# Optimization experiments

Hardware: AMD Instinct MI355X
Metric: run time of the kernel (lower is better)

Reference implementation:

```python
import jax, jax.numpy as jnp
import numpy as np

B, T, N, D, NH = 4, 256, 8, 128, 4
SCALES = (1, 2, 3, 5)
LAGS = (1, 2, 3)
MLP_H = 32
NL_SCALE = 0.1
CMIN, CMAX = -2.5, 2.0
L_ENC = 2  # num_attn_layers


def _ln(x, g, b, eps=1e-5):
    m = x.mean(-1, keepdims=True)
    v = ((x - m) ** 2).mean(-1, keepdims=True)
    return (x - m) * jax.lax.rsqrt(v + eps) * g + b


def _gelu(x):
    return jax.nn.gelu(x, approximate=False)


def _mha(q, k, v, Wq, bq, Wk, bk, Wv, bv, Wo, bo, nh):
    Bq, Lq, Dm = q.shape
    Lk = k.shape[1]
    hd = Dm // nh
    qh = (q @ Wq.T + bq).reshape(Bq, Lq, nh, hd).transpose(0, 2, 1, 3)
    kh = (k @ Wk.T + bk).reshape(Bq, Lk, nh, hd).transpose(0, 2, 1, 3)
    vh = (v @ Wv.T + bv).reshape(Bq, Lk, nh, hd).transpose(0, 2, 1, 3)
    s = jnp.einsum('bhqd,bhkd->bhqk', qh, kh) / jnp.sqrt(jnp.float32(hd))
    p = jax.nn.softmax(s, axis=-1)
    o = jnp.einsum('bhqk,bhkd->bhqd', p, vh).transpose(0, 2, 1, 3).reshape(Bq, Lq, Dm)
    return o @ Wo.T + bo


def setup_inputs() -> dict:
    key = jax.random.key(0)
    ks = jax.random.split(key, 24)
    def w(k, shape, s=0.02):
        return s * jax.random.normal(k, shape, jnp.float32)
    inp = {}
    inp['visible_states'] = jax.random.uniform(ks[0], (B, T, N), jnp.float32) + 0.05
    inp['state_emb'] = jax.random.normal(ks[1], (B, T, N, D), jnp.float32)
    # LearnedBaseline params
    inp['r5'] = 0.1 * jnp.ones((N,), jnp.float32)
    A = 0.02 * jax.random.normal(ks[2], (N, N), jnp.float32)
    inp['A55'] = A.at[jnp.arange(N), jnp.arange(N)].set(-0.2)
    inp['bl_bias'] = jnp.zeros((N,), jnp.float32)
    inp['nl_W1'] = w(ks[3], (MLP_H, N), 0.1); inp['nl_b1'] = jnp.zeros((MLP_H,), jnp.float32)
    inp['nl_W2'] = w(ks[4], (N, MLP_H), 0.1); inp['nl_b2'] = jnp.zeros((N,), jnp.float32)
    # ResidualEncoder input MLP
    IN_DIM = len(SCALES) * (1 + len(LAGS))  # 16
    inp['mlp_W1'] = w(ks[5], (D, IN_DIM), 0.1); inp['mlp_b1'] = jnp.zeros((D,), jnp.float32)
    inp['mlp_W2'] = w(ks[6], (D, D)); inp['mlp_b2'] = jnp.zeros((D,), jnp.float32)
    inp['mlp_ln_g'] = jnp.ones((D,), jnp.float32); inp['mlp_ln_b'] = jnp.zeros((D,), jnp.float32)
    # ResidualEncoder transformer layers (stacked over L_ENC layers)
    inp['enc_qkv_W'] = w(ks[7], (L_ENC, 3 * D, D)); inp['enc_qkv_b'] = jnp.zeros((L_ENC, 3 * D), jnp.float32)
    inp['enc_out_W'] = w(ks[8], (L_ENC, D, D)); inp['enc_out_b'] = jnp.zeros((L_ENC, D), jnp.float32)
    inp['enc_ln1_g'] = jnp.ones((L_ENC, D), jnp.float32); inp['enc_ln1_b'] = jnp.zeros((L_ENC, D), jnp.float32)
    inp['enc_ff_W1'] = w(ks[9], (L_ENC, 2 * D, D)); inp['enc_ff_b1'] = jnp.zeros((L_ENC, 2 * D), jnp.float32)
    inp['enc_ff_W2'] = w(ks[10], (L_ENC, D, 2 * D)); inp['enc_ff_b2'] = jnp.zeros((L_ENC, D), jnp.float32)
    inp['enc_ln2_g'] = jnp.ones((L_ENC, D), jnp.float32); inp['enc_ln2_b'] = jnp.zeros((L_ENC, D), jnp.float32)
    # CrossAttentionFusion
    inp['ca_Wq'] = w(ks[11], (D, D)); inp['ca_bq'] = jnp.zeros((D,), jnp.float32)
    inp['ca_Wk'] = w(ks[12], (D, D)); inp['ca_bk'] = jnp.zeros((D,), jnp.float32)
    inp['ca_Wv'] = w(ks[13], (D, D)); inp['ca_bv'] = jnp.zeros((D,), jnp.float32)
    inp['ca_Wo'] = w(ks[14], (D, D)); inp['ca_bo'] = jnp.zeros((D,), jnp.float32)
    inp['ca_ln1_g'] = jnp.ones((D,), jnp.float32); inp['ca_ln1_b'] = jnp.zeros((D,), jnp.float32)
    inp['ca_ff_W1'] = w(ks[15], (4 * D, 2 * D)); inp['ca_ff_b1'] = jnp.zeros((4 * D,), jnp.float32)
    inp['ca_ff_W2'] = w(ks[16], (D, 4 * D)); inp['ca_ff_b2'] = jnp.zeros((D,), jnp.float32)
    inp['ca_ln2_g'] = jnp.ones((D,), jnp.float32); inp['ca_ln2_b'] = jnp.zeros((D,), jnp.float32)
    return inp


def _forward(visible_states, state_emb, r5, A55, bl_bias, nl_W1, nl_b1, nl_W2, nl_b2,
             mlp_W1, mlp_b1, mlp_W2, mlp_b2, mlp_ln_g, mlp_ln_b,
             enc_qkv_W, enc_qkv_b, enc_out_W, enc_out_b, enc_ln1_g, enc_ln1_b,
             enc_ff_W1, enc_ff_b1, enc_ff_W2, enc_ff_b2, enc_ln2_g, enc_ln2_b,
             ca_Wq, ca_bq, ca_Wk, ca_bk, ca_Wv, ca_bv, ca_Wo, ca_bo,
             ca_ln1_g, ca_ln1_b, ca_ff_W1, ca_ff_b1, ca_ff_W2, ca_ff_b2,
             ca_ln2_g, ca_ln2_b):
    # ---- LearnedBaseline on x_t = visible_states[:, :-1] ----
    safe = jnp.clip(visible_states, 1e-6, None)
    logx = jnp.log(safe)
    x_t = visible_states[:, :-1]  # (B,T-1,N)
    lin = r5 + jnp.einsum('btn,mn->btm', x_t, A55)
    nl = _gelu(x_t @ nl_W1.T + nl_b1) @ nl_W2.T + nl_b2
    b1 = lin + NL_SCALE * nl + bl_bias  # (B,T-1,N)
    # ---- MultiScaleResidual ----
    res_list = []
    for k in SCALES:
        actual = jnp.clip(logx[:, k:] - logx[:, :-k], CMIN * k, CMAX * k)  # (B,T-k,N)
        bk = b1[:, 0:T - k]
        for i in range(1, k):
            bk = bk + b1[:, i:i + T - k]
        res = actual - bk
        res_list.append(jnp.pad(res, ((0, 0), (0, k), (0, 0))))
    residuals = jnp.stack(res_list, axis=-1)  # (B,T,N,S)
    # ---- ResidualEncoder: takens delays ----
    feats = [residuals] + [jnp.pad(residuals, ((0, 0), (lag, 0), (0, 0), (0, 0)))[:, :T]
                           for lag in LAGS]
    x = jnp.concatenate(feats, axis=-1)  # (B,T,N,16)
    x = _gelu(x @ mlp_W1.T + mlp_b1)
    x = _gelu(x @ mlp_W2.T + mlp_b2)
    x = _ln(x, mlp_ln_g, mlp_ln_b)
    # sinusoidal PE over time
    pos = jnp.arange(T, dtype=jnp.float32)[:, None]
    div = jnp.exp(jnp.arange(0, D, 2, dtype=jnp.float32) * (-jnp.log(10000.0) / D))
    pe = jnp.stack([jnp.sin(pos * div), jnp.cos(pos * div)], axis=-1).reshape(T, D)
    x = x + pe[None, :, None, :]
    # temporal self-attention over (B*N, T, D)
    xt = x.transpose(0, 2, 1, 3).reshape(B * N, T, D)
    for i in range(L_ENC):
        Wq, Wk, Wv = jnp.split(enc_qkv_W[i], 3, axis=0)
        bq, bk_, bv = jnp.split(enc_qkv_b[i], 3)
        a = _mha(xt, xt, xt, Wq, bq, Wk, bk_, Wv, bv, enc_out_W[i], enc_out_b[i], NH)
        xt = _ln(xt + a, enc_ln1_g[i], enc_ln1_b[i])
        ff = _gelu(xt @ enc_ff_W1[i].T + enc_ff_b1[i]) @ enc_ff_W2[i].T + enc_ff_b2[i]
        xt = _ln(xt + ff, enc_ln2_g[i], enc_ln2_b[i])
    residual_emb = xt.reshape(B, N, T, D).transpose(0, 2, 1, 3)  # (B,T,N,D)
    # ---- CrossAttentionFusion ----
    s = state_emb.reshape(B, T * N, D)
    r = residual_emb.reshape(B, T * N, D)
    a = _mha(s, r, r, ca_Wq, ca_bq, ca_Wk, ca_bk, ca_Wv, ca_bv, ca_Wo, ca_bo, NH)
    s = _ln(s + a, ca_ln1_g, ca_ln1_b)
    fused = _gelu(jnp.concatenate([s, r], axis=-1) @ ca_ff_W1.T + ca_ff_b1) @ ca_ff_W2.T + ca_ff_b2
    out = _ln(s + fused, ca_ln2_g, ca_ln2_b)
    return out.reshape(B, T, N, D)


def reference(visible_states, state_emb, r5, A55, bl_bias, nl_W1, nl_b1, nl_W2, nl_b2,
              mlp_W1, mlp_b1, mlp_W2, mlp_b2, mlp_ln_g, mlp_ln_b,
              enc_qkv_W, enc_qkv_b, enc_out_W, enc_out_b, enc_ln1_g, enc_ln1_b,
              enc_ff_W1, enc_ff_b1, enc_ff_W2, enc_ff_b2, enc_ln2_g, enc_ln2_b,
              ca_Wq, ca_bq, ca_Wk, ca_bk, ca_Wv, ca_bv, ca_Wo, ca_bo,
              ca_ln1_g, ca_ln1_b, ca_ff_W1, ca_ff_b1, ca_ff_W2, ca_ff_b2,
              ca_ln2_g, ca_ln2_b):
    return _forward(visible_states, state_emb, r5, A55, bl_bias, nl_W1, nl_b1, nl_W2, nl_b2,
                    mlp_W1, mlp_b1, mlp_W2, mlp_b2, mlp_ln_g, mlp_ln_b,
                    enc_qkv_W, enc_qkv_b, enc_out_W, enc_out_b, enc_ln1_g, enc_ln1_b,
                    enc_ff_W1, enc_ff_b1, enc_ff_W2, enc_ff_b2, enc_ln2_g, enc_ln2_b,
                    ca_Wq, ca_bq, ca_Wk, ca_bk, ca_Wv, ca_bv, ca_Wo, ca_bo,
                    ca_ln1_g, ca_ln1_b, ca_ff_W1, ca_ff_b1, ca_ff_W2, ca_ff_b2,
                    ca_ln2_g, ca_ln2_b)
```

## Files before the change

kernel.cpp:

```cpp
#include <hip/hip_runtime.h>
#include <math.h>

#define B_ 4
#define T_ 256
#define N_ 8
#define D_ 128
#define NH_ 4
#define HD_ 32
#define LENC_ 2
#define MLPH_ 32
#define NL_SCALE_ 0.1f

typedef __bf16 bf16;
typedef __attribute__((ext_vector_type(2))) __bf16 bf16x2;
typedef __attribute__((ext_vector_type(4))) __bf16 bf16x4;
typedef __attribute__((ext_vector_type(8))) __bf16 bf16x8;
typedef __attribute__((ext_vector_type(4))) float f32x4;

__device__ __forceinline__ f32x4 pv_mfma16(bf16x4 a, bf16x4 b, f32x4 c) {
#if __has_builtin(__builtin_amdgcn_mfma_f32_16x16x16_bf16)
    return __builtin_amdgcn_mfma_f32_16x16x16_bf16(a, b, c, 0, 0, 0);
#else
    typedef __attribute__((ext_vector_type(4))) short s4;
    union U { bf16x4 h; s4 s; };
    U ua, ub; ua.h = a; ub.h = b;
    return __builtin_amdgcn_mfma_f32_16x16x16bf16_1k(ua.s, ub.s, c, 0, 0, 0);
#endif
}

__device__ __forceinline__ float gelu_f(float x) {
    return 0.5f * x * (1.0f + erff(x * 0.7071067811865476f));
}

__device__ __forceinline__ float exp2_fast(float x) {
#if __has_builtin(__builtin_amdgcn_exp2f)
    return __builtin_amdgcn_exp2f(x);
#else
    return __expf(x * 0.6931471805599453f);
#endif
}

#define SCALE_LOG2E 0.25503486f

__global__ void k_prep_b1(const float* __restrict__ eqkvW, const float* __restrict__ eoutW,
                          const float* __restrict__ eff1, const float* __restrict__ eff2,
                          const float* __restrict__ wq, const float* __restrict__ wk,
                          const float* __restrict__ wv, const float* __restrict__ wo,
                          const float* __restrict__ cff1, const float* __restrict__ cff2,
                          const float* __restrict__ mlpW2, const float* __restrict__ semb,
                          const float* __restrict__ bk, const float* __restrict__ bv,
                          bf16* __restrict__ Wpk, bf16* __restrict__ sembh,
                          float* __restrict__ bpk,
                          const float* __restrict__ vs, const float* __restrict__ r5,
                          const float* __restrict__ A55, const float* __restrict__ bl_bias,
                          const float* __restrict__ nlW1, const float* __restrict__ nlb1,
                          const float* __restrict__ nlW2, const float* __restrict__ nlb2,
                          float* __restrict__ b1w) {
    if (blockIdx.x < 6209) {
        int i = blockIdx.x * 256 + threadIdx.x;
        if (i < 540672) {
            const float* src; int off;
            if      (i < 98304)  { src = eqkvW; off = 0; }
            else if (i < 131072) { src = eoutW; off = 98304; }
            else if (i < 196608) { src = eff1;  off = 131072; }
            else if (i < 262144) { src = eff2;  off = 196608; }
            else if (i < 278528) { src = wq;    off = 262144; }
            else if (i < 294912) { src = wk;    off = 278528; }
            else if (i < 311296) { src = wv;    off = 294912; }
            else if (i < 327680) { src = wo;    off = 311296; }
            else if (i < 458752) { src = cff1;  off = 327680; }
            else if (i < 524288) { src = cff2;  off = 458752; }
            else                 { src = mlpW2; off = 524288; }
            Wpk[i] = (bf16)src[i - off];
        } else if (i < 540672 + 1048576) {
            int j = i - 540672;
            sembh[j] = (bf16)semb[j];
        } else if (i < 540672 + 1048576 + 256) {
            int t = i - 540672 - 1048576;
            bpk[t] = (t < 128) ? bk[t] : bv[t - 128];
        }
        return;
    }
    int idx = (blockIdx.x - 6209) * 256 + threadIdx.x;
    if (idx >= B_ * (T_ - 1)) return;
    int b = idx / (T_ - 1), t = idx % (T_ - 1);
    float x[N_];
    for (int n = 0; n < N_; n++) x[n] = vs[(b * T_ + t) * N_ + n];
    float h[MLPH_];
    for (int j = 0; j < MLPH_; j++) {
        float a = nlb1[j];
        for (int n = 0; n < N_; n++) a += x[n] * nlW1[j * N_ + n];
        h[j] = gelu_f(a);
    }
    for (int m = 0; m < N_; m++) {
        float lin = r5[m];
        for (int n = 0; n < N_; n++) lin += x[n] * A55[m * N_ + n];
        float nl = nlb2[m];
        for (int j = 0; j < MLPH_; j++) nl += h[j] * nlW2[m * MLPH_ + j];
        b1w[idx * N_ + m] = lin + NL_SCALE_ * nl + bl_bias[m];
    }
}

__global__ __launch_bounds__(256) void k_mlp_ln(
    const float* __restrict__ vs, const float* __restrict__ b1w,
    const float* __restrict__ W1, const float* __restrict__ b1,
    const bf16* __restrict__ W2, const float* __restrict__ bias,
    const float* __restrict__ g, const float* __restrict__ be,
    float* __restrict__ outf, bf16* __restrict__ outh) {
    __shared__ float F[16][16];
    __shared__ bf16 H1[16][136];
    __shared__ float S[16][132];
    int tid = threadIdx.x;
    int blk = blockIdx.x;
    {
        int row = tid >> 4, feat = tid & 15;
        int grow = blk * 16 + row;
        int b = grow >> 11, t = (grow >> 3) & 255, n = grow & 7;
        const int SC[4] = {1, 2, 3, 5};
        int lag = feat >> 2, si = feat & 3, k = SC[si];
        int tp = t - lag;
        float r = 0.0f;
        if (tp >= 0 && tp < T_ - k) {
            float lx0 = logf(fmaxf(vs[(b * T_ + tp) * N_ + n], 1e-6f));
            float lx1 = logf(fmaxf(vs[(b * T_ + tp + k) * N_ + n], 1e-6f));
            float a = lx1 - lx0;
            a = fminf(fmaxf(a, -2.5f * (float)k), 2.0f * (float)k);
            float bk = 0.0f;
            for (int i = 0; i < k; i++) bk += b1w[(b * (T_ - 1) + tp + i) * N_ + n];
            r = a - bk;
        }
        F[row][feat] = r;
    }
    __syncthreads();
    {
        int row = tid >> 4, cg = tid & 15;
        float f[16];
#pragma unroll
        for (int c = 0; c < 16; c++) f[c] = F[row][c];
#pragma unroll
        for (int j = 0; j < 8; j++) {
            int d = cg * 8 + j;
            float a = b1[d];
            const float* w = W1 + d * 16;
#pragma unroll
            for (int c = 0; c < 16; c++) a += f[c] * w[c];
            H1[row][d] = (bf16)gelu_f(a);
        }
    }
    __syncthreads();
    int w = tid >> 6, lane = tid & 63;
    int c = lane & 15, gq = lane >> 4;
    int cb = w * 32;
    const f32x4 zero = {0, 0, 0, 0};
    {
        const bf16x8* Wp0 = (const bf16x8*)(W2 + (size_t)(cb + c) * 128) + gq;
        const bf16x8* Wp1 = (const bf16x8*)(W2 + (size_t)(cb + 16 + c) * 128) + gq;
        f32x4 a0 = zero, a1 = zero;
#pragma unroll
        for (int k = 0; k < 4; k++) {
            bf16x8 av = *(const bf16x8*)&H1[c][k * 32 + gq * 8];
            a0 = __builtin_amdgcn_mfma_f32_16x16x32_bf16(av, Wp0[k * 4], a0, 0, 0, 0);
            a1 = __builtin_amdgcn_mfma_f32_16x16x32_bf16(av, Wp1[k * 4], a1, 0, 0, 0);
        }
#pragma unroll
        for (int r = 0; r < 4; r++) {
            S[gq * 4 + r][cb + c]      = gelu_f(a0[r] + bias[cb + c]);
            S[gq * 4 + r][cb + 16 + c] = gelu_f(a1[r] + bias[cb + 16 + c]);
        }
    }
    __syncthreads();
    {
        int row = tid >> 4, cg = tid & 15;
        int grow = blk * 16 + row;
        int b = grow >> 11, t = (grow >> 3) & 255, n = grow & 7;
        int orow = (b * 8 + n) * 256 + t;
        float v[8];
#pragma unroll
        for (int j = 0; j < 8; j++) v[j] = S[row][cg * 8 + j];
        float s = 0.0f;
#pragma unroll
        for (int j = 0; j < 8; j++) s += v[j];
        s += __shfl_xor(s, 1); s += __shfl_xor(s, 2);
        s += __shfl_xor(s, 4); s += __shfl_xor(s, 8);
        float mean = s * (1.0f / 128.0f);
        float vs2 = 0.0f;
#pragma unroll
        for (int j = 0; j < 8; j++) { float d = v[j] - mean; vs2 += d * d; }
        vs2 += __shfl_xor(vs2, 1); vs2 += __shfl_xor(vs2, 2);
        vs2 += __shfl_xor(vs2, 4); vs2 += __shfl_xor(vs2, 8);
        float rstd = rsqrtf(vs2 * (1.0f / 128.0f) + 1e-5f);
        float y[8];
#pragma unroll
        for (int j = 0; j < 8; j++) {
            int col = cg * 8 + j;
            y[j] = (v[j] - mean) * rstd * g[col] + be[col];
        }
#pragma unroll
        for (int jj = 0; jj < 4; jj++) {
            int j2 = cg * 4 + jj;
            float freq = expf((float)(2 * j2) * (-9.210340371976184f / 128.0f));
            float ang = (float)t * freq;
            y[2 * jj] += sinf(ang);
            y[2 * jj + 1] += cosf(ang);
        }
        float4* of = (float4*)(outf + (size_t)orow * 128 + cg * 8);
        of[0] = (float4){y[0], y[1], y[2], y[3]};
        of[1] = (float4){y[4], y[5], y[6], y[7]};
        bf16x8 o;
#pragma unroll
        for (int e = 0; e < 8; e++) o[e] = (bf16)y[e];
        *(bf16x8*)(outh + (size_t)orow * 128 + cg * 8) = o;
    }
}

__global__ __launch_bounds__(256) void k_enc_attn(
    const bf16* __restrict__ X0h, const bf16* __restrict__ Wqkv,
    const float* __restrict__ bqkv, bf16* __restrict__ ATTh) {
    int sh = blockIdx.x & 127;
    int qh = blockIdx.x >> 7;
    int s = sh >> 2, h = sh & 3;
    __shared__ bf16 Ql[64][40];
    __shared__ bf16 Kl[256][40];
    __shared__ bf16 Vt[32][264];
    int tid = threadIdx.x;
    int wv = tid >> 6, lane = tid & 63;
    int c = lane & 15, g = lane >> 4;
    const f32x4 zero = {0, 0, 0, 0};

    const bf16* Wq0 = Wqkv + (size_t)(h * 32 + c) * 128;
    const bf16* Wq1 = Wqkv + (size_t)(h * 32 + 16 + c) * 128;
    const bf16* Wk0 = Wqkv + (size_t)(128 + h * 32 + c) * 128;
    const bf16* Wk1 = Wqkv + (size_t)(128 + h * 32 + 16 + c) * 128;
    const bf16* Wv0 = Wqkv + (size_t)(256 + h * 32 + c) * 128;
    const bf16* Wv1 = Wqkv + (size_t)(256 + h * 32 + 16 + c) * 128;
    float bq0 = bqkv[h * 32 + c], bq1 = bqkv[h * 32 + 16 + c];
    float bk0 = bqkv[128 + h * 32 + c], bk1 = bqkv[128 + h * 32 + 16 + c];
    float bv0 = bqkv[256 + h * 32 + c], bv1 = bqkv[256 + h * 32 + 16 + c];

#pragma unroll
    for (int rb = 0; rb < 4; rb++) {
        int row0 = wv * 64 + rb * 16;
        const bf16x8* Ap = (const bf16x8*)(X0h + (size_t)(s * 256 + row0 + c) * 128) + g;
        f32x4 ak0 = zero, ak1 = zero, av0 = zero, av1 = zero;
#pragma unroll
        for (int k = 0; k < 4; k++) {
            bf16x8 av = Ap[k * 4];
            ak0 = __builtin_amdgcn_mfma_f32_16x16x32_bf16(av, *((const bf16x8*)Wk0 + k * 4 + g), ak0, 0, 0, 0);
            ak1 = __builtin_amdgcn_mfma_f32_16x16x32_bf16(av, *((const bf16x8*)Wk1 + k * 4 + g), ak1, 0, 0, 0);
            av0 = __builtin_amdgcn_mfma_f32_16x16x32_bf16(av, *((const bf16x8*)Wv0 + k * 4 + g), av0, 0, 0, 0);
            av1 = __builtin_amdgcn_mfma_f32_16x16x32_bf16(av, *((const bf16x8*)Wv1 + k * 4 + g), av1, 0, 0, 0);
        }
        int lr = row0 + g * 4;
#pragma unroll
        for (int i = 0; i < 4; i++) {
            Kl[lr + i][c] = (bf16)(ak0[i] + bk0);
            Kl[lr + i][16 + c] = (bf16)(ak1[i] + bk1);
            Vt[c][lr + i] = (bf16)(av0[i] + bv0);
            Vt[16 + c][lr + i] = (bf16)(av1[i] + bv1);
        }
    }
    {
        int row0q = wv * 16;
        const bf16x8* Ap = (const bf16x8*)(
            X0h + (size_t)(s * 256 + qh * 64 + row0q + c) * 128) + g;
        f32x4 aq0 = zero, aq1 = zero;
#pragma unroll
        for (int k = 0; k < 4; k++) {
            bf16x8 av = Ap[k * 4];
            aq0 = __builtin_amdgcn_mfma_f32_16x16x32_bf16(av, *((const bf16x8*)Wq0 + k * 4 + g), aq0, 0, 0, 0);
            aq1 = __builtin_amdgcn_mfma_f32_16x16x32_bf16(av, *((const bf16x8*)Wq1 + k * 4 + g), aq1, 0, 0, 0);
        }
        int lr = row0q + g * 4;
#pragma unroll
        for (int i = 0; i < 4; i++) {
            Ql[lr + i][c] = (bf16)(aq0[i] + bq0);
            Ql[lr + i][16 + c] = (bf16)(aq1[i] + bq1);
        }
    }
    __syncthreads();

    int q0l = wv * 16;
    bf16x8 bqv = *(const bf16x8*)&Ql[q0l + c][g * 8];
    f32x4 oT0 = zero, oT1 = zero;
    float lsum = 0.0f;
#pragma unroll
    for (int t = 0; t < 8; t++) {
        int k0 = t * 32;
        bf16x8 ka = *(const bf16x8*)&Kl[k0 + c][g * 8];
        bf16x8 kb = *(const bf16x8*)&Kl[k0 + 16 + c][g * 8];
        bf16x4 va0 = *(const bf16x4*)&Vt[c][k0 + g * 4];
        bf16x4 va1 = *(const bf16x4*)&Vt[c][k0 + 16 + g * 4];
        bf16x4 vb0 = *(const bf16x4*)&Vt[16 + c][k0 + g * 4];
        bf16x4 vb1 = *(const bf16x4*)&Vt[16 + c][k0 + 16 + g * 4];
        f32x4 s0 = __builtin_amdgcn_mfma_f32_16x16x32_bf16(ka, bqv, zero, 0, 0, 0);
        f32x4 s1 = __builtin_amdgcn_mfma_f32_16x16x32_bf16(kb, bqv, zero, 0, 0, 0);
        bf16x4 p0, p1;
#pragma unroll
        for (int r = 0; r < 4; r++) {
            float e0 = exp2_fast(s0[r] * SCALE_LOG2E);
            float e1 = exp2_fast(s1[r] * SCALE_LOG2E);
            lsum += e0 + e1;
            p0[r] = (bf16)e0;
            p1[r] = (bf16)e1;
        }
        oT0 = pv_mfma16(va0, p0, oT0);
        oT0 = pv_mfma16(va1, p1, oT0);
        oT1 = pv_mfma16(vb0, p0, oT1);
        oT1 = pv_mfma16(vb1, p1, oT1);
    }
    {
        float sm = lsum;
        sm += __shfl_xor(sm, 16);
        sm += __shfl_xor(sm, 32);
        float inv = 1.0f / sm;
        size_t rbase = ((size_t)s * 256 + qh * 64 + q0l + c) * 128 + h * 32;
#pragma unroll
        for (int r = 0; r < 4; r++) {
            ATTh[rbase + g * 4 + r] = (bf16)(oT0[r] * inv);
            ATTh[rbase + 16 + g * 4 + r] = (bf16)(oT1[r] * inv);
        }
    }
}

__device__ __forceinline__ void gemm4_body(
    int bid, const bf16* __restrict__ A, const bf16* __restrict__ W,
    const float* __restrict__ bias, bf16* __restrict__ dq,
    bf16* __restrict__ dk, bf16* __restrict__ dvv, int N, int K, int mode) {
    int lane = threadIdx.x & 63;
    int wv = threadIdx.x >> 6;
    int c = lane & 15, g = lane >> 4;
    int nN = N >> 6;
    int tn = bid % nN, tm = bid / nN;
    int row0 = tm * 64 + wv * 16;
    int cb = tn * 64;

    const bf16x8* Ap  = (const bf16x8*)(A + (size_t)(row0 + c) * K) + g;
    const bf16x8* Wp0 = (const bf16x8*)(W + (size_t)(cb + c) * K) + g;
    const bf16x8* Wp1 = (const bf16x8*)(W + (size_t)(cb + 16 + c) * K) + g;
    const bf16x8* Wp2 = (const bf16x8*)(W + (size_t)(cb + 32 + c) * K) + g;
    const bf16x8* Wp3 = (const bf16x8*)(W + (size_t)(cb + 48 + c) * K) + g;
    f32x4 a0 = {0, 0, 0, 0}, a1 = {0, 0, 0, 0};
    f32x4 a2 = {0, 0, 0, 0}, a3 = {0, 0, 0, 0};
    int nk = K >> 5;
    for (int k = 0; k < nk; k++) {
        bf16x8 av = Ap[k * 4];
        a0 = __builtin_amdgcn_mfma_f32_16x16x32_bf16(av, Wp0[k * 4], a0, 0, 0, 0);
        a1 = __builtin_amdgcn_mfma_f32_16x16x32_bf16(av, Wp1[k * 4], a1, 0, 0, 0);
        a2 = __builtin_amdgcn_mfma_f32_16x16x32_bf16(av, Wp2[k * 4], a2, 0, 0, 0);
        a3 = __builtin_amdgcn_mfma_f32_16x16x32_bf16(av, Wp3[k * 4], a3, 0, 0, 0);
    }
    int rowb = row0 + g * 4;
#pragma unroll
    for (int ct = 0; ct < 4; ct++) {
        f32x4 acc = (ct == 0) ? a0 : (ct == 1) ? a1 : (ct == 2) ? a2 : a3;
        int col = cb + ct * 16 + c;
        float bvv = bias[col];
#pragma unroll
        for (int i = 0; i < 4; i++) {
            float v = acc[i] + bvv;
            int row = rowb + i;
            if (mode == 2) {
                int b = row >> 11, ll = row & 2047;
                int hh = col >> 5, d = col & 31;
                dq[((size_t)(b * 4 + hh) * 2048 + ll) * 32 + d] = (bf16)v;
            } else {
                int b = row >> 11, n = (row >> 8) & 7, t = row & 255;
                int ll = t * 8 + n;
                int hh = (col >> 5) & 3, d = col & 31;
                if (col < 128) dk[((size_t)(b * 4 + hh) * 2048 + ll) * 32 + d] = (bf16)v;
                else           dvv[((size_t)(b * 4 + hh) * 32 + d) * 2048 + ll] = (bf16)v;
            }
        }
    }
}

__global__ __launch_bounds__(256) void k_qkvc(
    const bf16* __restrict__ sembh, const bf16* __restrict__ Wq,
    const float* __restrict__ bq, const bf16* __restrict__ X0h,
    const bf16* __restrict__ Wkv, const float* __restrict__ bkv,
    bf16* __restrict__ Qh, bf16* __restrict__ Kh, bf16* __restrict__ Vth) {
    if (blockIdx.x < 256)
        gemm4_body(blockIdx.x, sembh, Wq, bq, Qh, nullptr, nullptr, 128, 128, 2);
    else
        gemm4_body(blockIdx.x - 256, X0h, Wkv, bkv, nullptr, Kh, Vth, 256, 128, 3);
}

__global__ __launch_bounds__(256) void k_enc_tail(
    const bf16* __restrict__ ATTh, const bf16* __restrict__ Wo,
    const float* __restrict__ bo, const float* __restrict__ X0res,
    const float* __restrict__ g1, const float* __restrict__ be1,
    const bf16* __restrict__ W1, const float* __restrict__ bf1,
    const bf16* __restrict__ W2, const float* __restrict__ bf2,
    const float* __restrict__ g2, const float* __restrict__ be2,
    float* __restrict__ X0out, bf16* __restrict__ X0hout) {
    __shared__ float S[16][132];
    __shared__ float X1f[16][132];
    __shared__ bf16 X1h[16][136];
    __shared__ bf16 H[16][264];
    int tid = threadIdx.x;
    int w = tid >> 6, lane = tid & 63;
    int c = lane & 15, gq = lane >> 4;
    int blk = blockIdx.x;
    const f32x4 zero = {0, 0, 0, 0};

    {
        int cb = w * 32;
        const bf16x8* Ap  = (const bf16x8*)(ATTh + (size_t)(blk * 16 + c) * 128) + gq;
        const bf16x8* Wp0 = (const bf16x8*)(Wo + (size_t)(cb + c) * 128) + gq;
        const bf16x8* Wp1 = (const bf16x8*)(Wo + (size_t)(cb + 16 + c) * 128) + gq;
        f32x4 a0 = zero, a1 = zero;
#pragma unroll
        for (int k = 0; k < 4; k++) {
            bf16x8 av = Ap[k * 4];
            a0 = __builtin_amdgcn_mfma_f32_16x16x32_bf16(av, Wp0[k * 4], a0, 0, 0, 0);
            a1 = __builtin_amdgcn_mfma_f32_16x16x32_bf16(av, Wp1[k * 4], a1, 0, 0, 0);
        }
#pragma unroll
        for (int r = 0; r < 4; r++) {
            S[gq * 4 + r][cb + c] = a0[r] + bo[cb + c];
            S[gq * 4 + r][cb + 16 + c] = a1[r] + bo[cb + 16 + c];
        }
    }
    __syncthreads();
    {
        int row = tid >> 4, cg = tid & 15;
        float v[8];
        const float4* rp = (const float4*)(X0res + (size_t)(blk * 16 + row) * 128 + cg * 8);
        float4 r0 = rp[0], r1 = rp[1];
        v[0] = S[row][cg * 8 + 0] + r0.x; v[1] = S[row][cg * 8 + 1] + r0.y;
        v[2] = S[row][cg * 8 + 2] + r0.z; v[3] = S[row][cg * 8 + 3] + r0.w;
        v[4] = S[row][cg * 8 + 4] + r1.x; v[5] = S[row][cg * 8 + 5] + r1.y;
        v[6] = S[row][cg * 8 + 6] + r1.z; v[7] = S[row][cg * 8 + 7] + r1.w;
        float s = 0.0f;
#pragma unroll
        for (int j = 0; j < 8; j++) s += v[j];
        s += __shfl_xor(s, 1); s += __shfl_xor(s, 2);
        s += __shfl_xor(s, 4); s += __shfl_xor(s, 8);
        float mean = s * (1.0f / 128.0f);
        float vs = 0.0f;
#pragma unroll
        for (int j = 0; j < 8; j++) { float d = v[j] - mean; vs += d * d; }
        vs += __shfl_xor(vs, 1); vs += __shfl_xor(vs, 2);
        vs += __shfl_xor(vs, 4); vs += __shfl_xor(vs, 8);
        float rstd = rsqrtf(vs * (1.0f / 128.0f) + 1e-5f);
#pragma unroll
        for (int j = 0; j < 8; j++) {
            int col = cg * 8 + j;
            float y = (v[j] - mean) * rstd * g1[col] + be1[col];
            X1f[row][col] = y;
            X1h[row][col] = (bf16)y;
        }
    }
    __syncthreads();
    {
        int cb2 = w * 64;
        bf16x8 af[4];
#pragma unroll
        for (int k = 0; k < 4; k++)
            af[k] = *(const bf16x8*)&X1h[c][k * 32 + gq * 8];
        const bf16x8* Wp0 = (const bf16x8*)(W1 + (size_t)(cb2 + c) * 128) + gq;
        const bf16x8* Wp1 = (const bf16x8*)(W1 + (size_t)(cb2 + 16 + c) * 128) + gq;
        const bf16x8* Wp2 = (const bf16x8*)(W1 + (size_t)(cb2 + 32 + c) * 128) + gq;
        const bf16x8* Wp3 = (const bf16x8*)(W1 + (size_t)(cb2 + 48 + c) * 128) + gq;
        f32x4 a0 = zero, a1 = zero, a2 = zero, a3 = zero;
#pragma unroll
        for (int k = 0; k < 4; k++) {
            a0 = __builtin_amdgcn_mfma_f32_16x16x32_bf16(af[k], Wp0[k * 4], a0, 0, 0, 0);
            a1 = __builtin_amdgcn_mfma_f32_16x16x32_bf16(af[k], Wp1[k * 4], a1, 0, 0, 0);
            a2 = __builtin_amdgcn_mfma_f32_16x16x32_bf16(af[k], Wp2[k * 4], a2, 0, 0, 0);
            a3 = __builtin_amdgcn_mfma_f32_16x16x32_bf16(af[k], Wp3[k * 4], a3, 0, 0, 0);
        }
#pragma unroll
        for (int r = 0; r < 4; r++) {
            H[gq * 4 + r][cb2 + c]      = (bf16)gelu_f(a0[r] + bf1[cb2 + c]);
            H[gq * 4 + r][cb2 + 16 + c] = (bf16)gelu_f(a1[r] + bf1[cb2 + 16 + c]);
            H[gq * 4 + r][cb2 + 32 + c] = (bf16)gelu_f(a2[r] + bf1[cb2 + 32 + c]);
            H[gq * 4 + r][cb2 + 48 + c] = (bf16)gelu_f(a3[r] + bf1[cb2 + 48 + c]);
        }
    }
    __syncthreads();
    {
        int cb = w * 32;
        bf16x8 af[8];
#pragma unroll
        for (int k = 0; k < 8; k++)
            af[k] = *(const bf16x8*)&H[c][k * 32 + gq * 8];
        const bf16x8* Wp0 = (const bf16x8*)(W2 + (size_t)(cb + c) * 256) + gq;
        const bf16x8* Wp1 = (const bf16x8*)(W2 + (size_t)(cb + 16 + c) * 256) + gq;
        f32x4 a0 = zero, a1 = zero;
#pragma unroll
        for (int k = 0; k < 8; k++) {
            a0 = __builtin_amdgcn_mfma_f32_16x16x32_bf16(af[k], Wp0[k * 4], a0, 0, 0, 0);
            a1 = __builtin_amdgcn_mfma_f32_16x16x32_bf16(af[k], Wp1[k * 4], a1, 0, 0, 0);
        }
#pragma unroll
        for (int r = 0; r < 4; r++) {
            S[gq * 4 + r][cb + c] = a0[r] + bf2[cb + c];
            S[gq * 4 + r][cb + 16 + c] = a1[r] + bf2[cb + 16 + c];
        }
    }
    __syncthreads();
    {
        int row = tid >> 4, cg = tid & 15;
        float v[8];
#pragma unroll
        for (int j = 0; j < 8; j++)
            v[j] = S[row][cg * 8 + j] + X1f[row][cg * 8 + j];
        float s = 0.0f;
#pragma unroll
        for (int j = 0; j < 8; j++) s += v[j];
        s += __shfl_xor(s, 1); s += __shfl_xor(s, 2);
        s += __shfl_xor(s, 4); s += __shfl_xor(s, 8);
        float mean = s * (1.0f / 128.0f);
        float vs = 0.0f;
#pragma unroll
        for (int j = 0; j < 8; j++) { float d = v[j] - mean; vs += d * d; }
        vs += __shfl_xor(vs, 1); vs += __shfl_xor(vs, 2);
        vs += __shfl_xor(vs, 4); vs += __shfl_xor(vs, 8);
        float rstd = rsqrtf(vs * (1.0f / 128.0f) + 1e-5f);
        size_t grow = (size_t)(blk * 16 + row);
        float y[8];
#pragma unroll
        for (int j = 0; j < 8; j++) {
            int col = cg * 8 + j;
            y[j] = (v[j] - mean) * rstd * g2[col] + be2[col];
        }
        float4* of = (float4*)(X0out + grow * 128 + cg * 8);
        of[0] = (float4){y[0], y[1], y[2], y[3]};
        of[1] = (float4){y[4], y[5], y[6], y[7]};
        bf16x8 o;
#pragma unroll
        for (int e = 0; e < 8; e++) o[e] = (bf16)y[e];
        *(bf16x8*)(X0hout + grow * 128 + cg * 8) = o;
    }
}

__global__ __launch_bounds__(256) void k_cross_tail(
    const bf16* __restrict__ ATTh, const bf16* __restrict__ Wo,
    const float* __restrict__ bo, const float* __restrict__ semb,
    const float* __restrict__ g1, const float* __restrict__ be1,
    const bf16* __restrict__ X0h, const bf16* __restrict__ W1,
    const float* __restrict__ bf1, const bf16* __restrict__ W2,
    const float* __restrict__ bf2, const float* __restrict__ g2,
    const float* __restrict__ be2, float* __restrict__ outp) {
    __shared__ float S[16][132];
    __shared__ bf16 s1h[16][136];
    __shared__ bf16 H[16][520];
    int tid = threadIdx.x;
    int w = tid >> 6, lane = tid & 63;
    int c = lane & 15, gq = lane >> 4;
    int blk = blockIdx.x;
    const f32x4 zero = {0, 0, 0, 0};

    bf16x8 agl[4];
    {
        int tr = blk * 16 + c;
        int b = tr >> 11, t = (tr >> 3) & 255, n = tr & 7;
        const bf16* xrow = X0h + ((size_t)((b * 8 + n) * 256 + t)) * 128;
#pragma unroll
        for (int k = 0; k < 4; k++)
            agl[k] = *(const bf16x8*)(xrow + k * 32 + gq * 8);
    }

    {
        int cb = w * 32;
        const bf16x8* Ap  = (const bf16x8*)(ATTh + (size_t)(blk * 16 + c) * 128) + gq;
        const bf16x8* Wp0 = (const bf16x8*)(Wo + (size_t)(cb + c) * 128) + gq;
        const bf16x8* Wp1 = (const bf16x8*)(Wo + (size_t)(cb + 16 + c) * 128) + gq;
        f32x4 a0 = zero, a1 = zero;
#pragma unroll
        for (int k = 0; k < 4; k++) {
            bf16x8 av = Ap[k * 4];
            a0 = __builtin_amdgcn_mfma_f32_16x16x32_bf16(av, Wp0[k * 4], a0, 0, 0, 0);
            a1 = __builtin_amdgcn_mfma_f32_16x16x32_bf16(av, Wp1[k * 4], a1, 0, 0, 0);
        }
#pragma unroll
        for (int r = 0; r < 4; r++) {
            S[gq * 4 + r][cb + c] = a0[r] + bo[cb + c];
            S[gq * 4 + r][cb + 16 + c] = a1[r] + bo[cb + 16 + c];
        }
    }
    __syncthreads();
    {
        int row = tid >> 4, cg = tid & 15;
        float v[8];
        const float4* rp = (const float4*)(semb + (size_t)(blk * 16 + row) * 128 + cg * 8);
        float4 r0 = rp[0], r1 = rp[1];
        v[0] = S[row][cg * 8 + 0] + r0.x; v[1] = S[row][cg * 8 + 1] + r0.y;
        v[2] = S[row][cg * 8 + 2] + r0.z; v[3] = S[row][cg * 8 + 3] + r0.w;
        v[4] = S[row][cg * 8 + 4] + r1.x; v[5] = S[row][cg * 8 + 5] + r1.y;
        v[6] = S[row][cg * 8 + 6] + r1.z; v[7] = S[row][cg * 8 + 7] + r1.w;
        float s = 0.0f;
#pragma unroll
        for (int j = 0; j < 8; j++) s += v[j];
        s += __shfl_xor(s, 1); s += __shfl_xor(s, 2);
        s += __shfl_xor(s, 4); s += __shfl_xor(s, 8);
        float mean = s * (1.0f / 128.0f);
        float vs = 0.0f;
#pragma unroll
        for (int j = 0; j < 8; j++) { float d = v[j] - mean; vs += d * d; }
        vs += __shfl_xor(vs, 1); vs += __shfl_xor(vs, 2);
        vs += __shfl_xor(vs, 4); vs += __shfl_xor(vs, 8);
        float rstd = rsqrtf(vs * (1.0f / 128.0f) + 1e-5f);
#pragma unroll
        for (int j = 0; j < 8; j++) {
            int col = cg * 8 + j;
            s1h[row][col] = (bf16)((v[j] - mean) * rstd * g1[col] + be1[col]);
        }
    }
    __syncthreads();
    {
        bf16x8 afl[4];
#pragma unroll
        for (int k = 0; k < 4; k++)
            afl[k] = *(const bf16x8*)&s1h[c][k * 32 + gq * 8];
#pragma unroll
        for (int ci = 0; ci < 2; ci++) {
            int cb2 = w * 128 + ci * 64;
            const bf16x8* Wp0 = (const bf16x8*)(W1 + (size_t)(cb2 + c) * 256) + gq;
            const bf16x8* Wp1 = (const bf16x8*)(W1 + (size_t)(cb2 + 16 + c) * 256) + gq;
            const bf16x8* Wp2 = (const bf16x8*)(W1 + (size_t)(cb2 + 32 + c) * 256) + gq;
            const bf16x8* Wp3 = (const bf16x8*)(W1 + (size_t)(cb2 + 48 + c) * 256) + gq;
            f32x4 a0 = zero, a1 = zero, a2 = zero, a3 = zero;
#pragma unroll
            for (int k = 0; k < 8; k++) {
                bf16x8 av = (k < 4) ? afl[k] : agl[k - 4];
                a0 = __builtin_amdgcn_mfma_f32_16x16x32_bf16(av, Wp0[k * 4], a0, 0, 0, 0);
                a1 = __builtin_amdgcn_mfma_f32_16x16x32_bf16(av, Wp1[k * 4], a1, 0, 0, 0);
                a2 = __builtin_amdgcn_mfma_f32_16x16x32_bf16(av, Wp2[k * 4], a2, 0, 0, 0);
                a3 = __builtin_amdgcn_mfma_f32_16x16x32_bf16(av, Wp3[k * 4], a3, 0, 0, 0);
            }
#pragma unroll
            for (int r = 0; r < 4; r++) {
                H[gq * 4 + r][cb2 + c]      = (bf16)gelu_f(a0[r] + bf1[cb2 + c]);
                H[gq * 4 + r][cb2 + 16 + c] = (bf16)gelu_f(a1[r] + bf1[cb2 + 16 + c]);
                H[gq * 4 + r][cb2 + 32 + c] = (bf16)gelu_f(a2[r] + bf1[cb2 + 32 + c]);
                H[gq * 4 + r][cb2 + 48 + c] = (bf16)gelu_f(a3[r] + bf1[cb2 + 48 + c]);
            }
        }
    }
    __syncthreads();
    {
        int cb = w * 32;
        const bf16x8* Wp0 = (const bf16x8*)(W2 + (size_t)(cb + c) * 512) + gq;
        const bf16x8* Wp1 = (const bf16x8*)(W2 + (size_t)(cb + 16 + c) * 512) + gq;
        f32x4 a0 = zero, a1 = zero;
#pragma unroll
        for (int k = 0; k < 16; k++) {
            bf16x8 av = *(const bf16x8*)&H[c][k * 32 + gq * 8];
            a0 = __builtin_amdgcn_mfma_f32_16x16x32_bf16(av, Wp0[k * 4], a0, 0, 0, 0);
            a1 = __builtin_amdgcn_mfma_f32_16x16x32_bf16(av, Wp1[k * 4], a1, 0, 0, 0);
        }
#pragma unroll
        for (int r = 0; r < 4; r++) {
            S[gq * 4 + r][cb + c] = a0[r] + bf2[cb + c];
            S[gq * 4 + r][cb + 16 + c] = a1[r] + bf2[cb + 16 + c];
        }
    }
    __syncthreads();
    {
        int row = tid >> 4, cg = tid & 15;
        float v[8];
#pragma unroll
        for (int j = 0; j < 8; j++)
            v[j] = S[row][cg * 8 + j] + (float)s1h[row][cg * 8 + j];
        float s = 0.0f;
#pragma unroll
        for (int j = 0; j < 8; j++) s += v[j];
        s += __shfl_xor(s, 1); s += __shfl_xor(s, 2);
        s += __shfl_xor(s, 4); s += __shfl_xor(s, 8);
        float mean = s * (1.0f / 128.0f);
        float vs = 0.0f;
#pragma unroll
        for (int j = 0; j < 8; j++) { float d = v[j] - mean; vs += d * d; }
        vs += __shfl_xor(vs, 1); vs += __shfl_xor(vs, 2);
        vs += __shfl_xor(vs, 4); vs += __shfl_xor(vs, 8);
        float rstd = rsqrtf(vs * (1.0f / 128.0f) + 1e-5f);
        float y[8];
#pragma unroll
        for (int j = 0; j < 8; j++) {
            int col = cg * 8 + j;
            y[j] = (v[j] - mean) * rstd * g2[col] + be2[col];
        }
        float4* of = (float4*)(outp + (size_t)(blk * 16 + (tid >> 4)) * 128 + cg * 8);
        of[0] = (float4){y[0], y[1], y[2], y[3]};
        of[1] = (float4){y[4], y[5], y[6], y[7]};
    }
}

__global__ __launch_bounds__(256) void k_mattn(
    const bf16* __restrict__ Qh, const bf16* __restrict__ Kh,
    const bf16* __restrict__ Vth, bf16* __restrict__ ATTh,
    int Lq, int Lk, int NSH) {
    int sh = blockIdx.x % NSH;
    int qblk = blockIdx.x / NSH;
    int wv = threadIdx.x >> 6;
    int lane = threadIdx.x & 63;
    int c = lane & 15, g = lane >> 4;
    int q0 = qblk * 64;

    __shared__ float O_lds[4][64][36];
    __shared__ float L_lds[4][64];

    const f32x4 zero = {0, 0, 0, 0};

    bf16x8 bq[4];
#pragma unroll
    for (int qt = 0; qt < 4; qt++)
        bq[qt] = *(const bf16x8*)(
            Qh + ((size_t)sh * Lq + q0 + qt * 16 + c) * 32 + g * 8);

    int klen = Lk >> 2;
    int kbeg = wv * klen;
    const bf16* Kbase = Kh + (size_t)sh * Lk * 32 + (size_t)kbeg * 32;
    const bf16* Vbase = Vth + (size_t)sh * 32 * Lk + kbeg;

    f32x4 oT[4][2];
#pragma unroll
    for (int qt = 0; qt < 4; qt++) { oT[qt][0] = zero; oT[qt][1] = zero; }
    float lsum[4] = {0, 0, 0, 0};

    int ntiles = klen >> 5;
    bf16x8 ka = *(const bf16x8*)(Kbase + (size_t)c * 32 + g * 8);
    bf16x8 kb = *(const bf16x8*)(Kbase + (size_t)(16 + c) * 32 + g * 8);
    bf16x4 va0 = *(const bf16x4*)(Vbase + (size_t)c * Lk + g * 4);
    bf16x4 va1 = *(const bf16x4*)(Vbase + (size_t)c * Lk + 16 + g * 4);
    bf16x4 vb0 = *(const bf16x4*)(Vbase + (size_t)(16 + c) * Lk + g * 4);
    bf16x4 vb1 = *(const bf16x4*)(Vbase + (size_t)(16 + c) * Lk + 16 + g * 4);

    for (int t = 0; t < ntiles; t++) {
        bf16x8 cka = ka, ckb = kb;
        bf16x4 cva0 = va0, cva1 = va1, cvb0 = vb0, cvb1 = vb1;
        int nk0 = ((t + 1 < ntiles) ? (t + 1) : t) << 5;
        ka = *(const bf16x8*)(Kbase + (size_t)(nk0 + c) * 32 + g * 8);
        kb = *(const bf16x8*)(Kbase + (size_t)(nk0 + 16 + c) * 32 + g * 8);
        va0 = *(const bf16x4*)(Vbase + (size_t)c * Lk + nk0 + g * 4);
        va1 = *(const bf16x4*)(Vbase + (size_t)c * Lk + nk0 + 16 + g * 4);
        vb0 = *(const bf16x4*)(Vbase + (size_t)(16 + c) * Lk + nk0 + g * 4);
        vb1 = *(const bf16x4*)(Vbase + (size_t)(16 + c) * Lk + nk0 + 16 + g * 4);

#pragma unroll
        for (int qt = 0; qt < 4; qt++) {
            f32x4 s0 = __builtin_amdgcn_mfma_f32_16x16x32_bf16(cka, bq[qt], zero, 0, 0, 0);
            f32x4 s1 = __builtin_amdgcn_mfma_f32_16x16x32_bf16(ckb, bq[qt], zero, 0, 0, 0);
            bf16x4 p0, p1;
#pragma unroll
            for (int r = 0; r < 4; r++) {
                float e0 = exp2_fast(s0[r] * SCALE_LOG2E);
                float e1 = exp2_fast(s1[r] * SCALE_LOG2E);
                lsum[qt] += e0 + e1;
                p0[r] = (bf16)e0;
                p1[r] = (bf16)e1;
            }
            oT[qt][0] = pv_mfma16(cva0, p0, oT[qt][0]);
            oT[qt][0] = pv_mfma16(cva1, p1, oT[qt][0]);
            oT[qt][1] = pv_mfma16(cvb0, p0, oT[qt][1]);
            oT[qt][1] = pv_mfma16(cvb1, p1, oT[qt][1]);
        }
    }

#pragma unroll
    for (int qt = 0; qt < 4; qt++) {
        float s = lsum[qt];
        s += __shfl_xor(s, 16);
        s += __shfl_xor(s, 32);
        if (g == 0) L_lds[wv][qt * 16 + c] = s;
        *(f32x4*)&O_lds[wv][qt * 16 + c][g * 4] = oT[qt][0];
        *(f32x4*)&O_lds[wv][qt * 16 + c][16 + g * 4] = oT[qt][1];
    }
    __syncthreads();

    int tid = threadIdx.x;
    int ql = tid >> 2, dq = (tid & 3) * 8;
    float ltot = L_lds[0][ql] + L_lds[1][ql] + L_lds[2][ql] + L_lds[3][ql];
    float inv = 1.0f / ltot;
    float acc[8];
#pragma unroll
    for (int j = 0; j < 8; j++) acc[j] = 0.0f;
#pragma unroll
    for (int w = 0; w < 4; w++) {
        const float* p = &O_lds[w][ql][dq];
#pragma unroll
        for (int j = 0; j < 8; j++) acc[j] += p[j];
    }
    int h = sh & 3, sb = sh >> 2;
    bf16x8 o;
#pragma unroll
    for (int j = 0; j < 8; j++) o[j] = (bf16)(acc[j] * inv);
    *(bf16x8*)(ATTh + ((size_t)sb * Lq + q0 + ql) * 128 + h * 32 + dq) = o;
}

extern "C" void kernel_launch(void* const* d_in, const int* in_sizes, int n_in,
                              void* d_out, int out_size, void* d_ws, size_t ws_size,
                              hipStream_t stream) {
    const float* vs       = (const float*)d_in[0];
    const float* semb     = (const float*)d_in[1];
    const float* r5       = (const float*)d_in[2];
    const float* A55      = (const float*)d_in[3];
    const float* bl_bias  = (const float*)d_in[4];
    const float* nl_W1    = (const float*)d_in[5];
    const float* nl_b1    = (const float*)d_in[6];
    const float* nl_W2    = (const float*)d_in[7];
    const float* nl_b2    = (const float*)d_in[8];
    const float* mlp_W1   = (const float*)d_in[9];
    const float* mlp_b1   = (const float*)d_in[10];
    const float* mlp_W2   = (const float*)d_in[11];
    const float* mlp_b2   = (const float*)d_in[12];
    const float* mlp_ln_g = (const float*)d_in[13];
    const float* mlp_ln_b = (const float*)d_in[14];
    const float* enc_qkv_W = (const float*)d_in[15];
    const float* enc_qkv_b = (const float*)d_in[16];
    const float* enc_out_W = (const float*)d_in[17];
    const float* enc_out_b = (const float*)d_in[18];
    const float* enc_ln1_g = (const float*)d_in[19];
    const float* enc_ln1_b = (const float*)d_in[20];
    const float* enc_ff_W1 = (const float*)d_in[21];
    const float* enc_ff_b1 = (const float*)d_in[22];
    const float* enc_ff_W2 = (const float*)d_in[23];
    const float* enc_ff_b2 = (const float*)d_in[24];
    const float* enc_ln2_g = (const float*)d_in[25];
    const float* enc_ln2_b = (const float*)d_in[26];
    const float* ca_Wq = (const float*)d_in[27];
    const float* ca_bq = (const float*)d_in[28];
    const float* ca_Wk = (const float*)d_in[29];
    const float* ca_bk = (const float*)d_in[30];
    const float* ca_Wv = (const float*)d_in[31];
    const float* ca_bv = (const float*)d_in[32];
    const float* ca_Wo = (const float*)d_in[33];
    const float* ca_bo = (const float*)d_in[34];
    const float* ca_ln1_g = (const float*)d_in[35];
    const float* ca_ln1_b = (const float*)d_in[36];
    const float* ca_ff_W1 = (const float*)d_in[37];
    const float* ca_ff_b1 = (const float*)d_in[38];
    const float* ca_ff_W2 = (const float*)d_in[39];
    const float* ca_ff_b2 = (const float*)d_in[40];
    const float* ca_ln2_g = (const float*)d_in[41];
    const float* ca_ln2_b = (const float*)d_in[42];
    float* out = (float*)d_out;

    char* base = (char*)d_ws;
    float* b1w   = (float*)(base + 0);
    float* X0    = (float*)(base + 163840);
    char*  QKVr  = base + 8552448;
    bf16*  Wpk   = (bf16*) (base + 25329664);
    float* bpk   = (float*)(base + 26411008);
    bf16*  X0h   = (bf16*) (base + 26412032);
    bf16*  sembh = (bf16*) (base + 30606336);
    bf16*  ATTh  = (bf16*) (base + 32703488);
    bf16*  Qh    = (bf16*)QKVr;
    bf16*  Kh    = (bf16*)(QKVr + 2097152);
    bf16*  Vth   = (bf16*)(QKVr + 4194304);

    k_prep_b1<<<dim3(6213), dim3(256), 0, stream>>>(
        enc_qkv_W, enc_out_W, enc_ff_W1, enc_ff_W2, ca_Wq, ca_Wk, ca_Wv, ca_Wo,
        ca_ff_W1, ca_ff_W2, mlp_W2, semb, ca_bk, ca_bv, Wpk, sembh, bpk,
        vs, r5, A55, bl_bias, nl_W1, nl_b1, nl_W2, nl_b2, b1w);

    k_mlp_ln<<<dim3(512), dim3(256), 0, stream>>>(
        vs, b1w, mlp_W1, mlp_b1, Wpk + 524288, mlp_b2, mlp_ln_g, mlp_ln_b,
        X0, X0h);

    for (int i = 0; i < LENC_; i++) {
        k_enc_attn<<<dim3(512), dim3(256), 0, stream>>>(
            X0h, Wpk + i * 49152, enc_qkv_b + i * 384, ATTh);
        k_enc_tail<<<dim3(512), dim3(256), 0, stream>>>(
            ATTh, Wpk + 98304 + i * 16384, enc_out_b + i * 128, X0,
            enc_ln1_g + i * 128, enc_ln1_b + i * 128,
            Wpk + 131072 + i * 32768, enc_ff_b1 + i * 256,
            Wpk + 196608 + i * 32768, enc_ff_b2 + i * 128,
            enc_ln2_g + i * 128, enc_ln2_b + i * 128, X0, X0h);
    }

    k_qkvc<<<dim3(768), dim3(256), 0, stream>>>(
        sembh, Wpk + 262144, ca_bq, X0h, Wpk + 278528, bpk, Qh, Kh, Vth);
    k_mattn<<<dim3(512), dim3(256), 0, stream>>>(
        Qh, Kh, Vth, ATTh, 2048, 2048, 16);
    k_cross_tail<<<dim3(512), dim3(256), 0, stream>>>(
        ATTh, Wpk + 311296, ca_bo, semb, ca_ln1_g, ca_ln1_b, X0h,
        Wpk + 327680, ca_ff_b1, Wpk + 458752, ca_ff_b2,
        ca_ln2_g, ca_ln2_b, out);
}
```

Before: 315.2 us.

## Fuse weight prep and baseline into MLP kernel, move Q projection into encoder tail

Merges the weight/embedding bf16 conversion and the learned-baseline computation into the input MLP kernel. Each block recomputes its local baseline window in shared memory instead of reading a global b1w buffer, and mlp_W2 is read as fp32 and converted inline. The cross-attention Q projection is folded into the last encoder-tail launch as extra blocks, with the softmax scale pre-multiplied into Q, so the score-side multiply is dropped. This removes launches and a dependency, at the cost of redundant baseline work per block and a grid-stride conversion loop inside the MLP kernel.

```diff
diff --git a/kernel.cpp b/kernel.cpp
--- a/kernel.cpp
+++ b/kernel.cpp
@@ -42,106 +42,115 @@
 
 #define SCALE_LOG2E 0.25503486f
 
-__global__ void k_prep_b1(const float* __restrict__ eqkvW, const float* __restrict__ eoutW,
-                          const float* __restrict__ eff1, const float* __restrict__ eff2,
-                          const float* __restrict__ wq, const float* __restrict__ wk,
-                          const float* __restrict__ wv, const float* __restrict__ wo,
-                          const float* __restrict__ cff1, const float* __restrict__ cff2,
-                          const float* __restrict__ mlpW2, const float* __restrict__ semb,
-                          const float* __restrict__ bk, const float* __restrict__ bv,
-                          bf16* __restrict__ Wpk, bf16* __restrict__ sembh,
-                          float* __restrict__ bpk,
-                          const float* __restrict__ vs, const float* __restrict__ r5,
-                          const float* __restrict__ A55, const float* __restrict__ bl_bias,
-                          const float* __restrict__ nlW1, const float* __restrict__ nlb1,
-                          const float* __restrict__ nlW2, const float* __restrict__ nlb2,
-                          float* __restrict__ b1w) {
-    if (blockIdx.x < 6209) {
-        int i = blockIdx.x * 256 + threadIdx.x;
-        if (i < 540672) {
-            const float* src; int off;
-            if      (i < 98304)  { src = eqkvW; off = 0; }
-            else if (i < 131072) { src = eoutW; off = 98304; }
-            else if (i < 196608) { src = eff1;  off = 131072; }
-            else if (i < 262144) { src = eff2;  off = 196608; }
-            else if (i < 278528) { src = wq;    off = 262144; }
-            else if (i < 294912) { src = wk;    off = 278528; }
-            else if (i < 311296) { src = wv;    off = 294912; }
-            else if (i < 327680) { src = wo;    off = 311296; }
-            else if (i < 458752) { src = cff1;  off = 327680; }
-            else if (i < 524288) { src = cff2;  off = 458752; }
-            else                 { src = mlpW2; off = 524288; }
-            Wpk[i] = (bf16)src[i - off];
-        } else if (i < 540672 + 1048576) {
-            int j = i - 540672;
-            sembh[j] = (bf16)semb[j];
-        } else if (i < 540672 + 1048576 + 256) {
-            int t = i - 540672 - 1048576;
-            bpk[t] = (t < 128) ? bk[t] : bv[t - 128];
-        }
-        return;
-    }
-    int idx = (blockIdx.x - 6209) * 256 + threadIdx.x;
-    if (idx >= B_ * (T_ - 1)) return;
-    int b = idx / (T_ - 1), t = idx % (T_ - 1);
-    float x[N_];
-    for (int n = 0; n < N_; n++) x[n] = vs[(b * T_ + t) * N_ + n];
-    float h[MLPH_];
-    for (int j = 0; j < MLPH_; j++) {
-        float a = nlb1[j];
-        for (int n = 0; n < N_; n++) a += x[n] * nlW1[j * N_ + n];
-        h[j] = gelu_f(a);
-    }
-    for (int m = 0; m < N_; m++) {
-        float lin = r5[m];
-        for (int n = 0; n < N_; n++) lin += x[n] * A55[m * N_ + n];
-        float nl = nlb2[m];
-        for (int j = 0; j < MLPH_; j++) nl += h[j] * nlW2[m * MLPH_ + j];
-        b1w[idx * N_ + m] = lin + NL_SCALE_ * nl + bl_bias[m];
-    }
-}
-
-__global__ __launch_bounds__(256) void k_mlp_ln(
-    const float* __restrict__ vs, const float* __restrict__ b1w,
-    const float* __restrict__ W1, const float* __restrict__ b1,
-    const bf16* __restrict__ W2, const float* __restrict__ bias,
-    const float* __restrict__ g, const float* __restrict__ be,
-    float* __restrict__ outf, bf16* __restrict__ outh) {
+__global__ __launch_bounds__(256) void k_mlp_prep(
+    const float* __restrict__ vs,
+    const float* __restrict__ mlpW1, const float* __restrict__ mlpb1,
+    const float* __restrict__ mlpW2f, const float* __restrict__ mlpb2,
+    const float* __restrict__ lng, const float* __restrict__ lnb,
+    const float* __restrict__ r5, const float* __restrict__ A55,
+    const float* __restrict__ bl_bias,
+    const float* __restrict__ nlW1, const float* __restrict__ nlb1,
+    const float* __restrict__ nlW2, const float* __restrict__ nlb2,
+    const float* __restrict__ eqkvW, const float* __restrict__ eoutW,
+    const float* __restrict__ eff1, const float* __restrict__ eff2,
+    const float* __restrict__ caWq, const float* __restrict__ caWk,
+    const float* __restrict__ caWv, const float* __restrict__ caWo,
+    const float* __restrict__ cff1, const float* __restrict__ cff2,
+    const float* __restrict__ semb, const float* __restrict__ cabk,
+    const float* __restrict__ cabv,
+    bf16* __restrict__ Wpk, bf16* __restrict__ sembh, float* __restrict__ bpk,
+    float* __restrict__ X0, bf16* __restrict__ X0h) {
     __shared__ float F[16][16];
+    __shared__ float b1loc[9][8];
     __shared__ bf16 H1[16][136];
     __shared__ float S[16][132];
     int tid = threadIdx.x;
     int blk = blockIdx.x;
+
+    {
+        const int NPK = 524288, NSB = 1048576;
+        for (int it = blk * 256 + tid; it < NPK + NSB + 256; it += 512 * 256) {
+            if (it < NPK) {
+                int i = it;
+                const float* src; int off;
+                if      (i < 98304)  { src = eqkvW; off = 0; }
+                else if (i < 131072) { src = eoutW; off = 98304; }
+                else if (i < 196608) { src = eff1;  off = 131072; }
+                else if (i < 262144) { src = eff2;  off = 196608; }
+                else if (i < 278528) { src = caWq;  off = 262144; }
+                else if (i < 294912) { src = caWk;  off = 278528; }
+                else if (i < 311296) { src = caWv;  off = 294912; }
+                else if (i < 327680) { src = caWo;  off = 311296; }
+                else if (i < 458752) { src = cff1;  off = 327680; }
+                else                 { src = cff2;  off = 458752; }
+                Wpk[i] = (bf16)src[i - off];
+            } else if (it < NPK + NSB) {
+                int j = it - NPK;
+                sembh[j] = (bf16)semb[j];
+            } else {
+                int t = it - NPK - NSB;
+                bpk[t] = (t < 128) ? cabk[t] : cabv[t - 128];
+            }
+        }
+    }
+
+    int t0 = (blk * 2) & 255;
+    int bB = blk >> 7;
+    if (tid < 72) {
+        int tt = t0 - 3 + (tid >> 3);
+        int m = tid & 7;
+        if (tt >= 0 && tt < T_ - 1) {
+            float x[N_];
+#pragma unroll
+            for (int n = 0; n < N_; n++) x[n] = vs[(bB * T_ + tt) * N_ + n];
+            float h[MLPH_];
+#pragma unroll
+            for (int j = 0; j < MLPH_; j++) {
+                float a = nlb1[j];
+#pragma unroll
+                for (int n = 0; n < N_; n++) a += x[n] * nlW1[j * N_ + n];
+                h[j] = gelu_f(a);
+            }
+            float lin = r5[m];
+#pragma unroll
+            for (int n = 0; n < N_; n++) lin += x[n] * A55[m * N_ + n];
+            float nl = nlb2[m];
+#pragma unroll
+            for (int j = 0; j < MLPH_; j++) nl += h[j] * nlW2[m * MLPH_ + j];
+            b1loc[tid >> 3][m] = lin + NL_SCALE_ * nl + bl_bias[m];
+        }
+    }
+    __syncthreads();
+
     {
         int row = tid >> 4, feat = tid & 15;
-        int grow = blk * 16 + row;
-        int b = grow >> 11, t = (grow >> 3) & 255, n = grow & 7;
+        int t = t0 + (row >> 3), n = row & 7;
         const int SC[4] = {1, 2, 3, 5};
         int lag = feat >> 2, si = feat & 3, k = SC[si];
         int tp = t - lag;
         float r = 0.0f;
         if (tp >= 0 && tp < T_ - k) {
-            float lx0 = logf(fmaxf(vs[(b * T_ + tp) * N_ + n], 1e-6f));
-            float lx1 = logf(fmaxf(vs[(b * T_ + tp + k) * N_ + n], 1e-6f));
+            float lx0 = logf(fmaxf(vs[(bB * T_ + tp) * N_ + n], 1e-6f));
+            float lx1 = logf(fmaxf(vs[(bB * T_ + tp + k) * N_ + n], 1e-6f));
             float a = lx1 - lx0;
             a = fminf(fmaxf(a, -2.5f * (float)k), 2.0f * (float)k);
             float bk = 0.0f;
-            for (int i = 0; i < k; i++) bk += b1w[(b * (T_ - 1) + tp + i) * N_ + n];
+            for (int i = 0; i < k; i++) bk += b1loc[tp + i - t0 + 3][n];
             r = a - bk;
         }
         F[row][feat] = r;
     }
     __syncthreads();
     {
-        int row = tid >> 4, cg = tid & 15;
+        int row = tid >> 4, cg_ = tid & 15;
         float f[16];
 #pragma unroll
         for (int c = 0; c < 16; c++) f[c] = F[row][c];
 #pragma unroll
         for (int j = 0; j < 8; j++) {
-            int d = cg * 8 + j;
-            float a = b1[d];
-            const float* w = W1 + d * 16;
+            int d = cg_ * 8 + j;
+            float a = mlpb1[d];
+            const float* w = mlpW1 + d * 16;
 #pragma unroll
             for (int c = 0; c < 16; c++) a += f[c] * w[c];
             H1[row][d] = (bf16)gelu_f(a);
@@ -153,30 +162,36 @@
     int cb = w * 32;
     const f32x4 zero = {0, 0, 0, 0};
     {
-        const bf16x8* Wp0 = (const bf16x8*)(W2 + (size_t)(cb + c) * 128) + gq;
-        const bf16x8* Wp1 = (const bf16x8*)(W2 + (size_t)(cb + 16 + c) * 128) + gq;
+        const float* w0 = mlpW2f + (size_t)(cb + c) * 128 + gq * 8;
+        const float* w1 = mlpW2f + (size_t)(cb + 16 + c) * 128 + gq * 8;
         f32x4 a0 = zero, a1 = zero;
 #pragma unroll
         for (int k = 0; k < 4; k++) {
             bf16x8 av = *(const bf16x8*)&H1[c][k * 32 + gq * 8];
-            a0 = __builtin_amdgcn_mfma_f32_16x16x32_bf16(av, Wp0[k * 4], a0, 0, 0, 0);
-            a1 = __builtin_amdgcn_mfma_f32_16x16x32_bf16(av, Wp1[k * 4], a1, 0, 0, 0);
+            bf16x8 wb0, wb1;
+#pragma unroll
+            for (int j = 0; j < 8; j++) {
+                wb0[j] = (bf16)w0[k * 32 + j];
+                wb1[j] = (bf16)w1[k * 32 + j];
+            }
+            a0 = __builtin_amdgcn_mfma_f32_16x16x32_bf16(av, wb0, a0, 0, 0, 0);
+            a1 = __builtin_amdgcn_mfma_f32_16x16x32_bf16(av, wb1, a1, 0, 0, 0);
         }
 #pragma unroll
         for (int r = 0; r < 4; r++) {
-            S[gq * 4 + r][cb + c]      = gelu_f(a0[r] + bias[cb + c]);
-            S[gq * 4 + r][cb + 16 + c] = gelu_f(a1[r] + bias[cb + 16 + c]);
-        }
-    }
-    __syncthreads();
-    {
-        int row = tid >> 4, cg = tid & 15;
+            S[gq * 4 + r][cb + c]      = gelu_f(a0[r] + mlpb2[cb + c]);
+            S[gq * 4 + r][cb + 16 + c] = gelu_f(a1[r] + mlpb2[cb + 16 + c]);
+        }
+    }
+    __syncthreads();
+    {
+        int row = tid >> 4, cg_ = tid & 15;
         int grow = blk * 16 + row;
         int b = grow >> 11, t = (grow >> 3) & 255, n = grow & 7;
         int orow = (b * 8 + n) * 256 + t;
         float v[8];
 #pragma unroll
-        for (int j = 0; j < 8; j++) v[j] = S[row][cg * 8 + j];
+        for (int j = 0; j < 8; j++) v[j] = S[row][cg_ * 8 + j];
         float s = 0.0f;
 #pragma unroll
         for (int j = 0; j < 8; j++) s += v[j];
@@ -192,24 +207,24 @@
         float y[8];
 #pragma unroll
         for (int j = 0; j < 8; j++) {
-            int col = cg * 8 + j;
-            y[j] = (v[j] - mean) * rstd * g[col] + be[col];
+            int col = cg_ * 8 + j;
+            y[j] = (v[j] - mean) * rstd * lng[col] + lnb[col];
         }
 #pragma unroll
         for (int jj = 0; jj < 4; jj++) {
-            int j2 = cg * 4 + jj;
+            int j2 = cg_ * 4 + jj;
             float freq = expf((float)(2 * j2) * (-9.210340371976184f / 128.0f));
             float ang = (float)t * freq;
             y[2 * jj] += sinf(ang);
             y[2 * jj + 1] += cosf(ang);
         }
-        float4* of = (float4*)(outf + (size_t)orow * 128 + cg * 8);
+        float4* of = (float4*)(X0 + (size_t)orow * 128 + cg_ * 8);
         of[0] = (float4){y[0], y[1], y[2], y[3]};
         of[1] = (float4){y[4], y[5], y[6], y[7]};
         bf16x8 o;
 #pragma unroll
         for (int e = 0; e < 8; e++) o[e] = (bf16)y[e];
-        *(bf16x8*)(outh + (size_t)orow * 128 + cg * 8) = o;
+        *(bf16x8*)(X0h + (size_t)orow * 128 + cg_ * 8) = o;
     }
 }
 
@@ -273,8 +288,8 @@
         int lr = row0q + g * 4;
 #pragma unroll
         for (int i = 0; i < 4; i++) {
-            Ql[lr + i][c] = (bf16)(aq0[i] + bq0);
-            Ql[lr + i][16 + c] = (bf16)(aq1[i] + bq1);
+            Ql[lr + i][c] = (bf16)((aq0[i] + bq0) * SCALE_LOG2E);
+            Ql[lr + i][16 + c] = (bf16)((aq1[i] + bq1) * SCALE_LOG2E);
         }
     }
     __syncthreads();
@@ -297,8 +312,8 @@
         bf16x4 p0, p1;
 #pragma unroll
         for (int r = 0; r < 4; r++) {
-            float e0 = exp2_fast(s0[r] * SCALE_LOG2E);
-            float e1 = exp2_fast(s1[r] * SCALE_LOG2E);
+            float e0 = exp2_fast(s0[r]);
+            float e1 = exp2_fast(s1[r]);
             lsum += e0 + e1;
             p0[r] = (bf16)e0;
             p1[r] = (bf16)e1;
@@ -325,7 +340,8 @@
 __device__ __forceinline__ void gemm4_body(
     int bid, const bf16* __restrict__ A, const bf16* __restrict__ W,
     const float* __restrict__ bias, bf16* __restrict__ dq,
-    bf16* __restrict__ dk, bf16* __restrict__ dvv, int N, int K, int mode) {
+    bf16* __restrict__ dk, bf16* __restrict__ dvv, int N, int K, int mode,
+    float qs) {
     int lane = threadIdx.x & 63;
     int wv = threadIdx.x >> 6;
     int c = lane & 15, g = lane >> 4;
@@ -360,6 +376,7 @@
             float v = acc[i] + bvv;
             int row = rowb + i;
             if (mode == 2) {
+                v *= qs;
                 int b = row >> 11, ll = row & 2047;
                 int hh = col >> 5, d = col & 31;
                 dq[((size_t)(b * 4 + hh) * 2048 + ll) * 32 + d] = (bf16)v;
@@ -374,17 +391,6 @@
     }
 }
 
-__global__ __launch_bounds__(256) void k_qkvc(
-    const bf16* __restrict__ sembh, const bf16* __restrict__ Wq,
-    const float* __restrict__ bq, const bf16* __restrict__ X0h,
-    const bf16* __restrict__ Wkv, const float* __restrict__ bkv,
-    bf16* __restrict__ Qh, bf16* __restrict__ Kh, bf16* __restrict__ Vth) {
-    if (blockIdx.x < 256)
-        gemm4_body(blockIdx.x, sembh, Wq, bq, Qh, nullptr, nullptr, 128, 128, 2);
-    else
-        gemm4_body(blockIdx.x - 256, X0h, Wkv, bkv, nullptr, Kh, Vth, 256, 128, 3);
-}
-
 __global__ __launch_bounds__(256) void k_enc_tail(
     const bf16* __restrict__ ATTh, const bf16* __restrict__ Wo,
     const float* __restrict__ bo, const float* __restrict__ X0res,
@@ -392,7 +398,14 @@
     const bf16* __restrict__ W1, const float* __restrict__ bf1,
     const bf16* __restrict__ W2, const float* __restrict__ bf2,
     const float* __restrict__ g2, const float* __restrict__ be2,
-    float* __restrict__ X0out, bf16* __restrict__ X0hout) {
+    float* __restrict__ X0out, bf16* __restrict__ X0hout,
+    const bf16* __restrict__ sembh, const bf16* __restrict__ Wq,
+    const float* __restrict__ bq, bf16* __restrict__ Qh) {
+    if (blockIdx.x >= 512) {
+        gemm4_body(blockIdx.x - 512, sembh, Wq, bq, Qh, nullptr, nullptr,
+                   128, 128, 2, SCALE_LOG2E);
+        return;
+    }
     __shared__ float S[16][132];
     __shared__ float X1f[16][132];
     __shared__ bf16 X1h[16][136];
@@ -423,14 +436,14 @@
     }
     __syncthreads();
     {
-        int row = tid >> 4, cg = tid & 15;
+        int row = tid >> 4, cg_ = tid & 15;
         float v[8];
-        const float4* rp = (const float4*)(X0res + (size_t)(blk * 16 + row) * 128 + cg * 8);
+        const float4* rp = (const float4*)(X0res + (size_t)(blk * 16 + row) * 128 + cg_ * 8);
         float4 r0 = rp[0], r1 = rp[1];
-        v[0] = S[row][cg * 8 + 0] + r0.x; v[1] = S[row][cg * 8 + 1] + r0.y;
-        v[2] = S[row][cg * 8 + 2] + r0.z; v[3] = S[row][cg * 8 + 3] + r0.w;
-        v[4] = S[row][cg * 8 + 4] + r1.x; v[5] = S[row][cg * 8 + 5] + r1.y;
-        v[6] = S[row][cg * 8 + 6] + r1.z; v[7] = S[row][cg * 8 + 7] + r1.w;
+        v[0] = S[row][cg_ * 8 + 0] + r0.x; v[1] = S[row][cg_ * 8 + 1] + r0.y;
+        v[2] = S[row][cg_ * 8 + 2] + r0.z; v[3] = S[row][cg_ * 8 + 3] + r0.w;
+        v[4] = S[row][cg_ * 8 + 4] + r1.x; v[5] = S[row][cg_ * 8 + 5] + r1.y;
+        v[6] = S[row][cg_ * 8 + 6] + r1.z; v[7] = S[row][cg_ * 8 + 7] + r1.w;
         float s = 0.0f;
 #pragma unroll
         for (int j = 0; j < 8; j++) s += v[j];
@@ -445,7 +458,7 @@
         float rstd = rsqrtf(vs * (1.0f / 128.0f) + 1e-5f);
 #pragma unroll
         for (int j = 0; j < 8; j++) {
-            int col = cg * 8 + j;
+            int col = cg_ * 8 + j;
             float y = (v[j] - mean) * rstd * g1[col] + be1[col];
             X1f[row][col] = y;
             X1h[row][col] = (bf16)y;
@@ -501,11 +514,11 @@
     }
     __syncthreads();
     {
-        int row = tid >> 4, cg = tid & 15;
+        int row = tid >> 4, cg_ = tid & 15;
         float v[8];
 #pragma unroll
         for (int j = 0; j < 8; j++)
-            v[j] = S[row][cg * 8 + j] + X1f[row][cg * 8 + j];
+            v[j] = S[row][cg_ * 8 + j] + X1f[row][cg_ * 8 + j];
         float s = 0.0f;
 #pragma unroll
         for (int j = 0; j < 8; j++) s += v[j];
@@ -522,17 +535,24 @@
         float y[8];
 #pragma unroll
         for (int j = 0; j < 8; j++) {
-            int col = cg * 8 + j;
+            int col = cg_ * 8 + j;
             y[j] = (v[j] - mean) * rstd * g2[col] + be2[col];
         }
-        float4* of = (float4*)(X0out + grow * 128 + cg * 8);
+        float4* of = (float4*)(X0out + grow * 128 + cg_ * 8);
         of[0] = (float4){y[0], y[1], y[2], y[3]};
         of[1] = (float4){y[4], y[5], y[6], y[7]};
         bf16x8 o;
 #pragma unroll
         for (int e = 0; e < 8; e++) o[e] = (bf16)y[e];
-        *(bf16x8*)(X0hout + grow * 128 + cg * 8) = o;
-    }
+        *(bf16x8*)(X0hout + grow * 128 + cg_ * 8) = o;
+    }
+}
+
+__global__ __launch_bounds__(256) void k_kv(
+    const bf16* __restrict__ X0h, const bf16* __restrict__ Wkv,
+    const float* __restrict__ bkv, bf16* __restrict__ Kh,
+    bf16* __restrict__ Vth) {
+    gemm4_body(blockIdx.x, X0h, Wkv, bkv, nullptr, Kh, Vth, 256, 128, 3, 1.0f);
 }
 
 __global__ __launch_bounds__(256) void k_cross_tail(
@@ -582,14 +602,14 @@
     }
     __syncthreads();
     {
-        int row = tid >> 4, cg = tid & 15;
+        int row = tid >> 4, cg_ = tid & 15;
         float v[8];
-        const float4* rp = (const float4*)(semb + (size_t)(blk * 16 + row) * 128 + cg * 8);
+        const float4* rp = (const float4*)(semb + (size_t)(blk * 16 + row) * 128 + cg_ * 8);
         float4 r0 = rp[0], r1 = rp[1];
-        v[0] = S[row][cg * 8 + 0] + r0.x; v[1] = S[row][cg * 8 + 1] + r0.y;
-        v[2] = S[row][cg * 8 + 2] + r0.z; v[3] = S[row][cg * 8 + 3] + r0.w;
-        v[4] = S[row][cg * 8 + 4] + r1.x; v[5] = S[row][cg * 8 + 5] + r1.y;
-        v[6] = S[row][cg * 8 + 6] + r1.z; v[7] = S[row][cg * 8 + 7] + r1.w;
+        v[0] = S[row][cg_ * 8 + 0] + r0.x; v[1] = S[row][cg_ * 8 + 1] + r0.y;
+        v[2] = S[row][cg_ * 8 + 2] + r0.z; v[3] = S[row][cg_ * 8 + 3] + r0.w;
+        v[4] = S[row][cg_ * 8 + 4] + r1.x; v[5] = S[row][cg_ * 8 + 5] + r1.y;
+        v[6] = S[row][cg_ * 8 + 6] + r1.z; v[7] = S[row][cg_ * 8 + 7] + r1.w;
         float s = 0.0f;
 #pragma unroll
         for (int j = 0; j < 8; j++) s += v[j];
@@ -604,7 +624,7 @@
         float rstd = rsqrtf(vs * (1.0f / 128.0f) + 1e-5f);
 #pragma unroll
         for (int j = 0; j < 8; j++) {
-            int col = cg * 8 + j;
+            int col = cg_ * 8 + j;
             s1h[row][col] = (bf16)((v[j] - mean) * rstd * g1[col] + be1[col]);
         }
     }
@@ -659,11 +679,11 @@
     }
     __syncthreads();
     {
-        int row = tid >> 4, cg = tid & 15;
+        int row = tid >> 4, cg_ = tid & 15;
         float v[8];
 #pragma unroll
         for (int j = 0; j < 8; j++)
-            v[j] = S[row][cg * 8 + j] + (float)s1h[row][cg * 8 + j];
+            v[j] = S[row][cg_ * 8 + j] + (float)s1h[row][cg_ * 8 + j];
         float s = 0.0f;
 #pragma unroll
         for (int j = 0; j < 8; j++) s += v[j];
@@ -679,10 +699,10 @@
         float y[8];
 #pragma unroll
         for (int j = 0; j < 8; j++) {
-            int col = cg * 8 + j;
+            int col = cg_ * 8 + j;
             y[j] = (v[j] - mean) * rstd * g2[col] + be2[col];
         }
-        float4* of = (float4*)(outp + (size_t)(blk * 16 + (tid >> 4)) * 128 + cg * 8);
+        float4* of = (float4*)(outp + (size_t)(blk * 16 + row) * 128 + cg_ * 8);
         of[0] = (float4){y[0], y[1], y[2], y[3]};
         of[1] = (float4){y[4], y[5], y[6], y[7]};
     }
@@ -746,8 +766,8 @@
             bf16x4 p0, p1;
 #pragma unroll
             for (int r = 0; r < 4; r++) {
-                float e0 = exp2_fast(s0[r] * SCALE_LOG2E);
-                float e1 = exp2_fast(s1[r] * SCALE_LOG2E);
+                float e0 = exp2_fast(s0[r]);
+                float e1 = exp2_fast(s1[r]);
                 lsum[qt] += e0 + e1;
                 p0[r] = (bf16)e0;
                 p1[r] = (bf16)e1;
@@ -839,7 +859,6 @@
     float* out = (float*)d_out;
 
     char* base = (char*)d_ws;
-    float* b1w   = (float*)(base + 0);
     float* X0    = (float*)(base + 163840);
     char*  QKVr  = base + 8552448;
     bf16*  Wpk   = (bf16*) (base + 25329664);
@@ -851,28 +870,29 @@
     bf16*  Kh    = (bf16*)(QKVr + 2097152);
     bf16*  Vth   = (bf16*)(QKVr + 4194304);
 
-    k_prep_b1<<<dim3(6213), dim3(256), 0, stream>>>(
-        enc_qkv_W, enc_out_W, enc_ff_W1, enc_ff_W2, ca_Wq, ca_Wk, ca_Wv, ca_Wo,
-        ca_ff_W1, ca_ff_W2, mlp_W2, semb, ca_bk, ca_bv, Wpk, sembh, bpk,
-        vs, r5, A55, bl_bias, nl_W1, nl_b1, nl_W2, nl_b2, b1w);
-
-    k_mlp_ln<<<dim3(512), dim3(256), 0, stream>>>(
-        vs, b1w, mlp_W1, mlp_b1, Wpk + 524288, mlp_b2, mlp_ln_g, mlp_ln_b,
-        X0, X0h);
+    k_mlp_prep<<<dim3(512), dim3(256), 0, stream>>>(
+        vs, mlp_W1, mlp_b1, mlp_W2, mlp_b2, mlp_ln_g, mlp_ln_b,
+        r5, A55, bl_bias, nl_W1, nl_b1, nl_W2, nl_b2,
+        enc_qkv_W, enc_out_W, enc_ff_W1, enc_ff_W2,
+        ca_Wq, ca_Wk, ca_Wv, ca_Wo, ca_ff_W1, ca_ff_W2,
+        semb, ca_bk, ca_bv,
+        Wpk, sembh, bpk, X0, X0h);
 
     for (int i = 0; i < LENC_; i++) {
         k_enc_attn<<<dim3(512), dim3(256), 0, stream>>>(
             X0h, Wpk + i * 49152, enc_qkv_b + i * 384, ATTh);
-        k_enc_tail<<<dim3(512), dim3(256), 0, stream>>>(
+        int tgrid = (i == LENC_ - 1) ? 768 : 512;
+        k_enc_tail<<<dim3(tgrid), dim3(256), 0, stream>>>(
             ATTh, Wpk + 98304 + i * 16384, enc_out_b + i * 128, X0,
             enc_ln1_g + i * 128, enc_ln1_b + i * 128,
             Wpk + 131072 + i * 32768, enc_ff_b1 + i * 256,
             Wpk + 196608 + i * 32768, enc_ff_b2 + i * 128,
-            enc_ln2_g + i * 128, enc_ln2_b + i * 128, X0, X0h);
-    }
-
-    k_qkvc<<<dim3(768), dim3(256), 0, stream>>>(
-        sembh, Wpk + 262144, ca_bq, X0h, Wpk + 278528, bpk, Qh, Kh, Vth);
+            enc_ln2_g + i * 128, enc_ln2_b + i * 128, X0, X0h,
+            sembh, Wpk + 262144, ca_bq, Qh);
+    }
+
+    k_kv<<<dim3(512), dim3(256), 0, stream>>>(
+        X0h, Wpk + 278528, bpk, Kh, Vth);
     k_mattn<<<dim3(512), dim3(256), 0, stream>>>(
         Qh, Kh, Vth, ATTh, 2048, 2048, 16);
     k_cross_tail<<<dim3(512), dim3(256), 0, stream>>>(
```

After: 313.6 us. About the same (-0.5%).
